# Optimization experiments

Measured on AMD Instinct MI355X. Metric: run time of the kernel, lower is better.

## Reference

```python
import jax, jax.numpy as jnp
import numpy as np

N = 100000
E = 3200000
D = 128


def spmm(row, col, val, x, n):
    # y[i] = sum_{e: row[e]==i} val[e] * x[col[e]]  -- COO SpMM via gather + segment_sum
    msgs = x[col] * val[:, None]          # [E, D]
    return jax.ops.segment_sum(msgs, row, num_segments=n)


def setup_inputs() -> dict:
    key = jax.random.key(0)
    ks = jax.random.split(key, 8)
    edge_row = jnp.sort(jax.random.randint(ks[0], (E,), 0, N))
    edge_col = jax.random.randint(ks[1], (E,), 0, N)
    edge_val = jax.random.uniform(ks[2], (E,), dtype=jnp.float32) / 32.0  # ~normalized laplacian weights
    selfloop_diag = jnp.ones((N,), dtype=jnp.float32)
    features = jax.random.normal(ks[3], (N, D), dtype=jnp.float32)
    W1 = jax.random.normal(ks[4], (D, D), dtype=jnp.float32) * 0.05
    b1 = jax.random.normal(ks[5], (D,), dtype=jnp.float32) * 0.05
    W2 = jax.random.normal(ks[6], (D, D), dtype=jnp.float32) * 0.05
    b2 = jax.random.normal(ks[7], (D,), dtype=jnp.float32) * 0.05
    return {"edge_row": edge_row, "edge_col": edge_col, "edge_val": edge_val,
            "selfloop_diag": selfloop_diag, "features": features,
            "W1": W1, "b1": b1, "W2": W2, "b2": b2}


def reference(edge_row, edge_col, edge_val, selfloop_diag, features, W1, b1, W2, b2):
    n = features.shape[0]
    Lx = spmm(edge_row, edge_col, edge_val, features, n)       # L @ features
    inter_feats = Lx * features                                 # elementwise mul
    L1x = Lx + selfloop_diag[:, None] * features                 # (L + I) @ features
    part1 = L1x @ W1.T + b1                                      # linear1
    part2 = spmm(edge_row, edge_col, edge_val, inter_feats, n) @ W2.T + b2  # linear2(L @ inter)
    return part1 + part2
```

## Files before the change

### kernel.cpp

```cpp
#include <hip/hip_runtime.h>

#define DD 128
#define DH 64

typedef unsigned int uint32;
typedef unsigned short ushort16;
typedef __attribute__((ext_vector_type(8))) short short8;
typedef __attribute__((ext_vector_type(4))) float f32x4;
typedef __attribute__((ext_vector_type(2))) float f32x2;

__device__ __forceinline__ uint32 pack_bf16(float a, float b) {
    uint32 ua = __builtin_bit_cast(uint32, a);
    uint32 ub = __builtin_bit_cast(uint32, b);
    ua = (ua + 0x7fffu + ((ua >> 16) & 1u)) >> 16;
    ub = (ub + 0x7fffu + ((ub >> 16) & 1u)) >> 16;
    return ua | (ub << 16);
}

#if __has_builtin(__builtin_amdgcn_cvt_pk_f32_fp8) && __has_builtin(__builtin_amdgcn_cvt_pk_fp8_f32)
#define FP8_HW 1
#else
#define FP8_HW 0
#endif

__device__ __forceinline__ float2 fp8x2_dec(uint32 u) {
#if FP8_HW
    f32x2 r = __builtin_amdgcn_cvt_pk_f32_fp8(u, false);
    return make_float2(r.x, r.y);
#else
    float2 o;
    uint32 b0 = u & 0xff, b1 = (u >> 8) & 0xff;
    {
        uint32 s = (b0 >> 7) & 1, e = (b0 >> 3) & 15, m = b0 & 7;
        float v = (e == 0) ? ldexpf((float)m, -9) : ldexpf((float)(8 + m), (int)e - 10);
        o.x = s ? -v : v;
    }
    {
        uint32 s = (b1 >> 7) & 1, e = (b1 >> 3) & 15, m = b1 & 7;
        float v = (e == 0) ? ldexpf((float)m, -9) : ldexpf((float)(8 + m), (int)e - 10);
        o.y = s ? -v : v;
    }
    return o;
#endif
}

#if !FP8_HW
__device__ __forceinline__ uint32 fp8_enc1(float x) {
    uint32 u = __builtin_bit_cast(uint32, x);
    uint32 s = (u >> 31) << 7;
    float ax = fabsf(x);
    if (ax >= 448.f) return s | 0x7E;
    if (ax < 0.0009765625f) return s;
    if (ax >= 0.015625f) {
        uint32 e = (u >> 23) & 0xFF;
        uint32 m = u & 0x7FFFFF;
        uint32 keep = m >> 20, rest = m & 0xFFFFF;
        keep += (rest > 0x80000u) || (rest == 0x80000u && (keep & 1));
        uint32 ee = e - 127 + 7;
        if (keep == 8) { keep = 0; ee += 1; }
        if (ee > 15 || (ee == 15 && keep > 6)) return s | 0x7E;
        return s | (ee << 3) | keep;
    }
    uint32 ni = (uint32)(ax * 512.f + 0.5f);
    if (ni >= 8) return s | (1u << 3);
    return s | ni;
}
#endif

__device__ __forceinline__ uint32 fp8x2_enc(float a, float b) {
#if FP8_HW
    return __builtin_amdgcn_cvt_pk_fp8_f32(a, b, 0, false) & 0xffffu;
#else
    return fp8_enc1(a) | (fp8_enc1(b) << 8);
#endif
}

__device__ __forceinline__ uint32 fp8x4_enc(float4 f) {
#if FP8_HW
    uint32 w = __builtin_amdgcn_cvt_pk_fp8_f32(f.x, f.y, 0, false);
    w = __builtin_amdgcn_cvt_pk_fp8_f32(f.z, f.w, w, true);
    return w;
#else
    return fp8_enc1(f.x) | (fp8_enc1(f.y) << 8) | (fp8_enc1(f.z) << 16) | (fp8_enc1(f.w) << 24);
#endif
}

__global__ __launch_bounds__(256) void k_row_ptr(const int* __restrict__ row,
                                                 int* __restrict__ rp, int n, int e) {
    int i = blockIdx.x * 256 + threadIdx.x;
    if (i > n) return;
    int lo = 0, hi = e;
    while (lo < hi) { int m = (lo + hi) >> 1; if (row[m] < i) lo = m + 1; else hi = m; }
    rp[i] = lo;
}

__global__ __launch_bounds__(256) void k_prep(const float* __restrict__ feat,
                                              uint32* __restrict__ featq,
                                              const float* __restrict__ W1,
                                              const float* __restrict__ W2,
                                              uint32* __restrict__ Wb1,
                                              uint32* __restrict__ Wb2, int n) {
    int id = blockIdx.x * 256 + threadIdx.x;
    if (id < n * (DD / 4)) {
        float4 f = ((const float4*)feat)[id];
        featq[id] = fp8x4_enc(f);
    }
    if (id < 2 * DD * DD / 4) {
        int mat = id >> 12, rem = id & 4095;
        float4 wv = ((const float4*)(mat ? W2 : W1))[rem];
        uint2 p;
        p.x = pack_bf16(wv.x, wv.y);
        p.y = pack_bf16(wv.z, wv.w);
        ((uint2*)(mat ? Wb2 : Wb1))[rem] = p;
    }
}

template <int PASS>
__global__ __launch_bounds__(256) void k_spmm(const int* __restrict__ col,
                                              const float* __restrict__ val,
                                              const ushort16* __restrict__ xq,
                                              const int* __restrict__ rp,
                                              const float* __restrict__ feat,
                                              const float* __restrict__ diag,
                                              uint32* __restrict__ out1,
                                              ushort16* __restrict__ out2, int n) {
    int lane = threadIdx.x & 63;
    int row = blockIdx.x * 4 + (threadIdx.x >> 6);
    if (row >= n) return;
    row = __builtin_amdgcn_readfirstlane(row);
    int s = rp[row], eend = rp[row + 1];
    float ax = 0.f, ay = 0.f;
    int e = s;
    for (; e + 8 <= eend; e += 8) {
        int c[8]; float v[8]; ushort16 g[8];
#pragma unroll
        for (int u = 0; u < 8; ++u) { c[u] = col[e + u]; v[u] = val[e + u]; }
#pragma unroll
        for (int u = 0; u < 8; ++u) { g[u] = xq[c[u] * DH + lane]; }
#pragma unroll
        for (int u = 0; u < 8; ++u) {
            float2 f = fp8x2_dec(g[u]);
            ax = fmaf(v[u], f.x, ax);
            ay = fmaf(v[u], f.y, ay);
        }
    }
    for (; e < eend; ++e) {
        int c = col[e]; float v = val[e];
        float2 f = fp8x2_dec(xq[c * DH + lane]);
        ax = fmaf(v, f.x, ax);
        ay = fmaf(v, f.y, ay);
    }
    if (PASS == 1) {
        float dg = diag[row];
        float2 f = ((const float2*)feat)[(size_t)row * DH + lane];
        out1[row * DH + lane] = pack_bf16(fmaf(dg, f.x, ax), fmaf(dg, f.y, ay));
        out2[row * DH + lane] = (ushort16)fp8x2_enc(ax * f.x, ay * f.y);
    } else {
        out1[row * DH + lane] = pack_bf16(ax, ay);
    }
}

__global__ __launch_bounds__(512, 2) void k_gemm(const uint32* __restrict__ Abf,
                                                 const uint32* __restrict__ Bbf,
                                                 const uint32* __restrict__ Wb1g,
                                                 const uint32* __restrict__ Wb2g,
                                                 const float* __restrict__ b1,
                                                 const float* __restrict__ b2,
                                                 float* __restrict__ out, int n) {
    __shared__ __align__(16) char lds[65536];
    int t = threadIdx.x;
    {
        const uint2* s1 = (const uint2*)Wb1g;
        const uint2* s2 = (const uint2*)Wb2g;
#pragma unroll
        for (int u = 0; u < 16; ++u) {
            int id = u * 512 + t;
            int j = id >> 5, kq = id & 31;
            int dst = j * 256 + ((kq * 8) ^ ((j & 7) << 4));
            *(uint2*)(lds + dst) = s1[id];
            *(uint2*)(lds + 32768 + dst) = s2[id];
        }
    }
    __syncthreads();
    int lane = t & 63, w = t >> 6;
    int g = lane >> 4;
    int rowbase = blockIdx.x * 256 + w * 32;
    int rr = rowbase + (lane & 15);
    int r0 = min(rr, n - 1);
    int r1 = min(rr + 16, n - 1);
    const uint4* A4 = (const uint4*)Abf;
    const uint4* B4 = (const uint4*)Bbf;

    f32x4 acc[2][8];
#pragma unroll
    for (int mt = 0; mt < 2; ++mt)
#pragma unroll
        for (int jt = 0; jt < 8; ++jt) acc[mt][jt] = (f32x4){0.f, 0.f, 0.f, 0.f};

    uint4 a0 = A4[(size_t)r0 * 16 + g], a1 = A4[(size_t)r1 * 16 + g];
    uint4 c0 = B4[(size_t)r0 * 16 + g], c1 = B4[(size_t)r1 * 16 + g];
#pragma unroll
    for (int kc = 0; kc < 4; ++kc) {
        uint4 na0, na1, nc0, nc1;
        if (kc < 3) {
            na0 = A4[(size_t)r0 * 16 + (kc + 1) * 4 + g];
            na1 = A4[(size_t)r1 * 16 + (kc + 1) * 4 + g];
            nc0 = B4[(size_t)r0 * 16 + (kc + 1) * 4 + g];
            nc1 = B4[(size_t)r1 * 16 + (kc + 1) * 4 + g];
        }
        short8 fa0 = __builtin_bit_cast(short8, a0);
        short8 fa1 = __builtin_bit_cast(short8, a1);
        short8 fc0 = __builtin_bit_cast(short8, c0);
        short8 fc1 = __builtin_bit_cast(short8, c1);
        int kbase = kc * 64 + g * 16;
#pragma unroll
        for (int jt = 0; jt < 8; ++jt) {
            int j = jt * 16 + (lane & 15);
            int off = j * 256 + (kbase ^ ((j & 7) << 4));
            short8 w1 = *(const short8*)(lds + off);
            short8 w2 = *(const short8*)(lds + 32768 + off);
            acc[0][jt] = __builtin_amdgcn_mfma_f32_16x16x32_bf16(fa0, w1, acc[0][jt], 0, 0, 0);
            acc[0][jt] = __builtin_amdgcn_mfma_f32_16x16x32_bf16(fc0, w2, acc[0][jt], 0, 0, 0);
            acc[1][jt] = __builtin_amdgcn_mfma_f32_16x16x32_bf16(fa1, w1, acc[1][jt], 0, 0, 0);
            acc[1][jt] = __builtin_amdgcn_mfma_f32_16x16x32_bf16(fc1, w2, acc[1][jt], 0, 0, 0);
        }
        a0 = na0; a1 = na1; c0 = nc0; c1 = nc1;
    }
    float bsum[8];
#pragma unroll
    for (int jt = 0; jt < 8; ++jt) {
        int cj = jt * 16 + (lane & 15);
        bsum[jt] = b1[cj] + b2[cj];
    }
#pragma unroll
    for (int mt = 0; mt < 2; ++mt) {
#pragma unroll
        for (int i = 0; i < 4; ++i) {
            int r = rowbase + mt * 16 + g * 4 + i;
            if (r < n) {
                float* orow = out + (size_t)r * DD;
#pragma unroll
                for (int jt = 0; jt < 8; ++jt)
                    orow[jt * 16 + (lane & 15)] = acc[mt][jt][i] + bsum[jt];
            }
        }
    }
}

extern "C" void kernel_launch(void* const* d_in, const int* in_sizes, int n_in,
                              void* d_out, int out_size, void* d_ws, size_t ws_size,
                              hipStream_t stream) {
    const int*   edge_row = (const int*)d_in[0];
    const int*   edge_col = (const int*)d_in[1];
    const float* edge_val = (const float*)d_in[2];
    const float* diag     = (const float*)d_in[3];
    const float* feat     = (const float*)d_in[4];
    const float* W1       = (const float*)d_in[5];
    const float* b1       = (const float*)d_in[6];
    const float* W2       = (const float*)d_in[7];
    const float* b2       = (const float*)d_in[8];
    float* out = (float*)d_out;

    const int E = in_sizes[0];
    const int N = in_sizes[3];

    char* ws = (char*)d_ws;
    size_t off = 0;
    int* rp            = (int*)(ws + off);      off += (((size_t)(N + 1) * 4) + 255) & ~(size_t)255;
    uint32* featq      = (uint32*)(ws + off);   off += (size_t)N * (DD / 4) * 4;
    uint32* interq     = (uint32*)(ws + off);   off += (size_t)N * (DD / 4) * 4;
    uint32* L1xbf      = (uint32*)(ws + off);   off += (size_t)N * DH * 4;
    uint32* Linterbf   = (uint32*)(ws + off);   off += (size_t)N * DH * 4;
    uint32* Wb1g       = (uint32*)(ws + off);   off += (size_t)DD * DH * 4;
    uint32* Wb2g       = (uint32*)(ws + off);   off += (size_t)DD * DH * 4;
    (void)ws_size; (void)n_in; (void)out_size;

    k_row_ptr<<<(N + 1 + 255) / 256, 256, 0, stream>>>(edge_row, rp, N, E);
    {
        int work = N * (DD / 4);
        if (work < 2 * DD * DD / 4) work = 2 * DD * DD / 4;
        k_prep<<<(work + 255) / 256, 256, 0, stream>>>(feat, featq, W1, W2, Wb1g, Wb2g, N);
    }
    k_spmm<1><<<(N + 3) / 4, 256, 0, stream>>>(edge_col, edge_val, (const ushort16*)featq, rp,
                                               feat, diag, L1xbf, (ushort16*)interq, N);
    k_spmm<2><<<(N + 3) / 4, 256, 0, stream>>>(edge_col, edge_val, (const ushort16*)interq, rp,
                                               nullptr, nullptr, Linterbf, nullptr, N);
    k_gemm<<<(N + 255) / 256, 512, 0, stream>>>(L1xbf, Linterbf, Wb1g, Wb2g, b1, b2, out, N);
}
```

Baseline: 194.0 us.

## Split each SpMM wavefront into four edge groups with wider fp8 gathers

The SpMM kernel now splits each 64-lane wavefront into four 16-lane subgroups. Each subgroup handles a different edge and loads 8 fp8 features per lane as a uint2, rather than every lane loading 2 features per edge. Partial sums are combined with cross-lane shuffles, and 16 lanes write vectorized bf16/fp8 outputs. The aim is to issue wider gather loads and keep several edges in flight per row, in exchange for shuffle reductions, masked tail edges and fewer active lanes during the writeback.

Measured after the change: 247.0 us. 1.27x slower.

```diff
diff --git a/kernel.cpp b/kernel.cpp
--- a/kernel.cpp
+++ b/kernel.cpp
@@ -4,7 +4,6 @@
 #define DH 64
 
 typedef unsigned int uint32;
-typedef unsigned short ushort16;
 typedef __attribute__((ext_vector_type(8))) short short8;
 typedef __attribute__((ext_vector_type(4))) float f32x4;
 typedef __attribute__((ext_vector_type(2))) float f32x2;
@@ -23,28 +22,12 @@
 #define FP8_HW 0
 #endif
 
-__device__ __forceinline__ float2 fp8x2_dec(uint32 u) {
-#if FP8_HW
-    f32x2 r = __builtin_amdgcn_cvt_pk_f32_fp8(u, false);
-    return make_float2(r.x, r.y);
-#else
-    float2 o;
-    uint32 b0 = u & 0xff, b1 = (u >> 8) & 0xff;
-    {
-        uint32 s = (b0 >> 7) & 1, e = (b0 >> 3) & 15, m = b0 & 7;
-        float v = (e == 0) ? ldexpf((float)m, -9) : ldexpf((float)(8 + m), (int)e - 10);
-        o.x = s ? -v : v;
-    }
-    {
-        uint32 s = (b1 >> 7) & 1, e = (b1 >> 3) & 15, m = b1 & 7;
-        float v = (e == 0) ? ldexpf((float)m, -9) : ldexpf((float)(8 + m), (int)e - 10);
-        o.y = s ? -v : v;
-    }
-    return o;
-#endif
-}
-
 #if !FP8_HW
+__device__ __forceinline__ float fp8_dec1(uint32 b) {
+    uint32 s = (b >> 7) & 1, e = (b >> 3) & 15, m = b & 7;
+    float v = (e == 0) ? ldexpf((float)m, -9) : ldexpf((float)(8 + m), (int)e - 10);
+    return s ? -v : v;
+}
 __device__ __forceinline__ uint32 fp8_enc1(float x) {
     uint32 u = __builtin_bit_cast(uint32, x);
     uint32 s = (u >> 31) << 7;
@@ -67,11 +50,14 @@
 }
 #endif
 
-__device__ __forceinline__ uint32 fp8x2_enc(float a, float b) {
+template <bool WORD>
+__device__ __forceinline__ float2 fp8x2_dec(uint32 u) {
 #if FP8_HW
-    return __builtin_amdgcn_cvt_pk_fp8_f32(a, b, 0, false) & 0xffffu;
+    f32x2 r = __builtin_amdgcn_cvt_pk_f32_fp8(u, WORD);
+    return make_float2(r.x, r.y);
 #else
-    return fp8_enc1(a) | (fp8_enc1(b) << 8);
+    uint32 v = WORD ? (u >> 16) : u;
+    return make_float2(fp8_dec1(v & 0xff), fp8_dec1((v >> 8) & 0xff));
 #endif
 }
 
@@ -118,45 +104,74 @@
 template <int PASS>
 __global__ __launch_bounds__(256) void k_spmm(const int* __restrict__ col,
                                               const float* __restrict__ val,
-                                              const ushort16* __restrict__ xq,
+                                              const uint2* __restrict__ xq,
                                               const int* __restrict__ rp,
                                               const float* __restrict__ feat,
                                               const float* __restrict__ diag,
-                                              uint32* __restrict__ out1,
-                                              ushort16* __restrict__ out2, int n) {
+                                              uint4* __restrict__ out1,
+                                              uint2* __restrict__ out2, int n) {
     int lane = threadIdx.x & 63;
     int row = blockIdx.x * 4 + (threadIdx.x >> 6);
     if (row >= n) return;
     row = __builtin_amdgcn_readfirstlane(row);
     int s = rp[row], eend = rp[row + 1];
-    float ax = 0.f, ay = 0.f;
-    int e = s;
-    for (; e + 8 <= eend; e += 8) {
-        int c[8]; float v[8]; ushort16 g[8];
-#pragma unroll
-        for (int u = 0; u < 8; ++u) { c[u] = col[e + u]; v[u] = val[e + u]; }
-#pragma unroll
-        for (int u = 0; u < 8; ++u) { g[u] = xq[c[u] * DH + lane]; }
+    int sub = lane >> 4, d16 = lane & 15;
+    float acc[8];
+#pragma unroll
+    for (int k = 0; k < 8; ++k) acc[k] = 0.f;
+
+    for (int e = s; e < eend; e += 32) {
+        uint2 g[8]; float vv[8];
 #pragma unroll
         for (int u = 0; u < 8; ++u) {
-            float2 f = fp8x2_dec(g[u]);
-            ax = fmaf(v[u], f.x, ax);
-            ay = fmaf(v[u], f.y, ay);
-        }
-    }
-    for (; e < eend; ++e) {
-        int c = col[e]; float v = val[e];
-        float2 f = fp8x2_dec(xq[c * DH + lane]);
-        ax = fmaf(v, f.x, ax);
-        ay = fmaf(v, f.y, ay);
-    }
-    if (PASS == 1) {
-        float dg = diag[row];
-        float2 f = ((const float2*)feat)[(size_t)row * DH + lane];
-        out1[row * DH + lane] = pack_bf16(fmaf(dg, f.x, ax), fmaf(dg, f.y, ay));
-        out2[row * DH + lane] = (ushort16)fp8x2_enc(ax * f.x, ay * f.y);
-    } else {
-        out1[row * DH + lane] = pack_bf16(ax, ay);
+            int ee = e + u * 4 + sub;
+            int ec = min(ee, eend - 1);
+            int c = col[ec];
+            vv[u] = (ee < eend) ? val[ec] : 0.f;
+            g[u] = xq[(size_t)c * 16 + d16];
+        }
+#pragma unroll
+        for (int u = 0; u < 8; ++u) {
+            float v = vv[u];
+            float2 p0 = fp8x2_dec<false>(g[u].x);
+            float2 p1 = fp8x2_dec<true>(g[u].x);
+            float2 p2 = fp8x2_dec<false>(g[u].y);
+            float2 p3 = fp8x2_dec<true>(g[u].y);
+            acc[0] = fmaf(v, p0.x, acc[0]); acc[1] = fmaf(v, p0.y, acc[1]);
+            acc[2] = fmaf(v, p1.x, acc[2]); acc[3] = fmaf(v, p1.y, acc[3]);
+            acc[4] = fmaf(v, p2.x, acc[4]); acc[5] = fmaf(v, p2.y, acc[5]);
+            acc[6] = fmaf(v, p3.x, acc[6]); acc[7] = fmaf(v, p3.y, acc[7]);
+        }
+    }
+#pragma unroll
+    for (int k = 0; k < 8; ++k) {
+        acc[k] += __shfl_xor(acc[k], 16, 64);
+        acc[k] += __shfl_xor(acc[k], 32, 64);
+    }
+    if (lane < 16) {
+        if (PASS == 1) {
+            float dg = diag[row];
+            const float4* f4 = (const float4*)feat;
+            float4 f0 = f4[(size_t)row * 32 + d16 * 2];
+            float4 f1 = f4[(size_t)row * 32 + d16 * 2 + 1];
+            uint4 o;
+            o.x = pack_bf16(fmaf(dg, f0.x, acc[0]), fmaf(dg, f0.y, acc[1]));
+            o.y = pack_bf16(fmaf(dg, f0.z, acc[2]), fmaf(dg, f0.w, acc[3]));
+            o.z = pack_bf16(fmaf(dg, f1.x, acc[4]), fmaf(dg, f1.y, acc[5]));
+            o.w = pack_bf16(fmaf(dg, f1.z, acc[6]), fmaf(dg, f1.w, acc[7]));
+            out1[(size_t)row * 16 + d16] = o;
+            uint2 q;
+            q.x = fp8x4_enc(make_float4(acc[0] * f0.x, acc[1] * f0.y, acc[2] * f0.z, acc[3] * f0.w));
+            q.y = fp8x4_enc(make_float4(acc[4] * f1.x, acc[5] * f1.y, acc[6] * f1.z, acc[7] * f1.w));
+            out2[(size_t)row * 16 + d16] = q;
+        } else {
+            uint4 o;
+            o.x = pack_bf16(acc[0], acc[1]);
+            o.y = pack_bf16(acc[2], acc[3]);
+            o.z = pack_bf16(acc[4], acc[5]);
+            o.w = pack_bf16(acc[6], acc[7]);
+            out1[(size_t)row * 16 + d16] = o;
+        }
     }
 }
 
@@ -281,9 +296,9 @@
         if (work < 2 * DD * DD / 4) work = 2 * DD * DD / 4;
         k_prep<<<(work + 255) / 256, 256, 0, stream>>>(feat, featq, W1, W2, Wb1g, Wb2g, N);
     }
-    k_spmm<1><<<(N + 3) / 4, 256, 0, stream>>>(edge_col, edge_val, (const ushort16*)featq, rp,
-                                               feat, diag, L1xbf, (ushort16*)interq, N);
-    k_spmm<2><<<(N + 3) / 4, 256, 0, stream>>>(edge_col, edge_val, (const ushort16*)interq, rp,
-                                               nullptr, nullptr, Linterbf, nullptr, N);
+    k_spmm<1><<<(N + 3) / 4, 256, 0, stream>>>(edge_col, edge_val, (const uint2*)featq, rp,
+                                               feat, diag, (uint4*)L1xbf, (uint2*)interq, N);
+    k_spmm<2><<<(N + 3) / 4, 256, 0, stream>>>(edge_col, edge_val, (const uint2*)interq, rp,
+                                               nullptr, nullptr, (uint4*)Linterbf, nullptr, N);
     k_gemm<<<(N + 255) / 256, 512, 0, stream>>>(L1xbf, Linterbf, Wb1g, Wb2g, b1, b2, out, N);
 }
```
